# Performance work log

Hardware: AMD Instinct MI355X
Metric: run time of the kernel (lower is better)

Reference implementation:

```python
import jax, jax.numpy as jnp
import numpy as np

D_MODEL = 1024
N_HEADS = 16
LATENT_HEADS = 8
LATENT_DIM = 512
N_LATENTS = 64
WINDOW = 256
HEAD_DIM = D_MODEL // N_HEADS          # 64
LAT_HD = LATENT_DIM // LATENT_HEADS    # 64
B, S = 2, 4096


def setup_inputs() -> dict:
    key = jax.random.key(0)
    ks = jax.random.split(key, 11)
    std = 0.02
    w = lambda k, shp: jax.random.normal(k, shp, jnp.float32) * std
    return {
        'x': jax.random.normal(ks[0], (B, S, D_MODEL), jnp.float32),
        'wq': w(ks[1], (D_MODEL, D_MODEL)),
        'wk': w(ks[2], (D_MODEL, D_MODEL)),
        'wv': w(ks[3], (D_MODEL, D_MODEL)),
        'wgq': w(ks[4], (D_MODEL, LATENT_DIM)),
        'wgk': w(ks[5], (D_MODEL, LATENT_DIM)),
        'wgv': w(ks[6], (D_MODEL, LATENT_DIM)),
        'r_out_w': w(ks[7], (LATENT_DIM, D_MODEL)),
        'gate_local_w': w(ks[8], (N_HEADS, HEAD_DIM)),
        'gate_remote_w': w(ks[9], (N_HEADS, HEAD_DIM)),
        'w_out': w(ks[10], (D_MODEL, D_MODEL)),
    }


def _pool_to_latents(x):
    # x: [B, S, C]; S assumed divisible by N_LATENTS (matches torch path when S % chunk == 0)
    Bx, Sx, C = x.shape
    chunk = max(1, Sx // N_LATENTS)
    return x.reshape(Bx, N_LATENTS, chunk, C).mean(axis=2)  # [B, Nl, C]


def _local_window_attn(Q, K, V):
    # causal sliding-window attention: query i attends keys in [i-WINDOW+1, i]
    Bx, H, Sx, D = Q.shape
    W = WINDOW
    nb = Sx // W
    Qb = Q.reshape(Bx, H, nb, W, D)
    # pad one leading block of keys/values so block b sees key blocks (b-1, b)
    Kp = jnp.pad(K, ((0, 0), (0, 0), (W, 0), (0, 0))).reshape(Bx, H, nb + 1, W, D)
    Vp = jnp.pad(V, ((0, 0), (0, 0), (W, 0), (0, 0))).reshape(Bx, H, nb + 1, W, D)
    Kw = jnp.concatenate([Kp[:, :, :-1], Kp[:, :, 1:]], axis=3)  # [B,H,nb,2W,D]
    Vw = jnp.concatenate([Vp[:, :, :-1], Vp[:, :, 1:]], axis=3)
    i = jnp.arange(W)[:, None]
    j = jnp.arange(2 * W)[None, :]
    # key_pos <= q_pos  <=> j <= i+W ; key_pos >= q_pos-W+1 <=> j > i
    base = (j > i) & (j <= i + W)                       # [W, 2W]
    blk0 = (jnp.arange(nb) > 0)[:, None, None] | (j >= W)[None, :, :]  # pad keys invalid in block 0
    mask = base[None, :, :] & blk0                      # [nb, W, 2W]
    sc = jnp.einsum('bhnid,bhnjd->bhnij', Qb, Kw) / np.sqrt(D).astype(np.float32)
    sc = jnp.where(mask[None, None], sc, -jnp.inf)
    p = jax.nn.softmax(sc, axis=-1)
    out = jnp.einsum('bhnij,bhnjd->bhnid', p, Vw)
    return out.reshape(Bx, H, Sx, D)


def reference(x, wq, wk, wv, wgq, wgk, wgv, r_out_w, gate_local_w, gate_remote_w, w_out):
    Bx, Sx, _ = x.shape
    chunk = max(1, Sx // N_LATENTS)
    # local path projections: [B, H, S, Dh]
    Q = (x @ wq).reshape(Bx, Sx, N_HEADS, HEAD_DIM).transpose(0, 2, 1, 3)
    K = (x @ wk).reshape(Bx, Sx, N_HEADS, HEAD_DIM).transpose(0, 2, 1, 3)
    V = (x @ wv).reshape(Bx, Sx, N_HEADS, HEAD_DIM).transpose(0, 2, 1, 3)
    local = _local_window_attn(Q, K, V)                 # [B, H, S, Dh]
    # latent (remote) path: GQ over mean-pooled latents, chunk-causal
    GQ = (x @ wgq).reshape(Bx, Sx, LATENT_HEADS, LAT_HD).transpose(0, 2, 1, 3)   # [B,Lh,S,Ld]
    GK = _pool_to_latents(x @ wgk).reshape(Bx, N_LATENTS, LATENT_HEADS, LAT_HD).transpose(0, 2, 1, 3)
    GV = _pool_to_latents(x @ wgv).reshape(Bx, N_LATENTS, LATENT_HEADS, LAT_HD).transpose(0, 2, 1, 3)
    lsc = jnp.einsum('bhsd,bhnd->bhsn', GQ, GK) / np.sqrt(LAT_HD).astype(np.float32)
    lmask = jnp.arange(N_LATENTS)[None, :] <= (jnp.arange(Sx) // chunk)[:, None]  # [S, Nl]
    lsc = jnp.where(lmask[None, None], lsc, -jnp.inf)
    lp = jax.nn.softmax(lsc, axis=-1)
    rem = jnp.einsum('bhsn,bhnd->bhsd', lp, GV)          # [B, Lh, S, Ld]
    rem = rem.transpose(0, 2, 1, 3).reshape(Bx, Sx, LATENT_DIM) @ r_out_w  # [B, S, d_model]
    rem = rem.reshape(Bx, Sx, N_HEADS, HEAD_DIM).transpose(0, 2, 1, 3)     # [B, H, S, Dh]
    # learned per-head gates computed from the query
    gl = jax.nn.sigmoid(jnp.einsum('bhsd,hd->bhs', Q, gate_local_w))[..., None]
    gr = jax.nn.sigmoid(jnp.einsum('bhsd,hd->bhs', Q, gate_remote_w))[..., None]
    out = gl * local + gr * rem                          # [B, H, S, Dh]
    out = out.transpose(0, 2, 1, 3).reshape(Bx, Sx, D_MODEL)
    return out @ w_out
```

## Files before the change

kernel.cpp:

```cpp
#include <hip/hip_runtime.h>

#define AS1 __attribute__((address_space(1)))
#define AS3 __attribute__((address_space(3)))

typedef float    f32x4  __attribute__((ext_vector_type(4)));
typedef __bf16   bf16x8 __attribute__((ext_vector_type(8)));
typedef __bf16   bf16x4 __attribute__((ext_vector_type(4)));
typedef unsigned int u32x4 __attribute__((ext_vector_type(4)));

static constexpr int SEQ = 4096, NBATCH = 2, DMODEL = 1024, NHEADS = 16, HDIM = 64;
static constexpr int LHEADS = 8, LDIM = 512, NLAT = 64, WIN = 256;
static constexpr int BSROWS = NBATCH * SEQ;
static constexpr int QKVN = 3584;
static constexpr int KOFF = 1024, VOFF = 2048, GQOFF = 3072;

struct TJ { const float* in; __bf16* out; int K; int N; };
struct TJ8 { TJ j[8]; };
__global__ __launch_bounds__(256) void prep_all(const float* __restrict__ x,
                                                __bf16* __restrict__ xb,
                                                __bf16* __restrict__ xpool, TJ8 jobs) {
    __shared__ float tbuf[32][33];
    int bid = blockIdx.x, t = threadIdx.x;
    if (bid < 512) {
        int bn = bid >> 2;
        int c  = (bid & 3) * 256 + t;
        const float* p = x + (size_t)bn * 64 * 1024 + c;
        __bf16* q = xb + (size_t)bn * 64 * 1024 + c;
        float s = 0.f;
        #pragma unroll 8
        for (int j = 0; j < 64; ++j) {
            float v = p[(size_t)j * 1024];
            q[(size_t)j * 1024] = (__bf16)v;
            s += v;
        }
        xpool[(size_t)bn * 1024 + c] = (__bf16)(s * 0.015625f);
    } else if (bid < 8704) {
        int ti = bid - 512;
        TJ jb = jobs.j[ti >> 10];
        int rem = ti & 1023;
        int k0 = (rem >> 5) * 32, n0 = (rem & 31) * 32;
        if (k0 >= jb.K || n0 >= jb.N) return;
        int tx = t & 31, ty = t >> 5;
        #pragma unroll
        for (int i = ty; i < 32; i += 8) tbuf[i][tx] = jb.in[(size_t)(k0 + i) * jb.N + n0 + tx];
        __syncthreads();
        #pragma unroll
        for (int i = ty; i < 32; i += 8) jb.out[(size_t)(n0 + i) * jb.K + k0 + tx] = (__bf16)tbuf[tx][i];
    } else {
        int zi = bid - 8704;
        size_t idx = ((size_t)zi * 256 + t) * 16;
        u32x4 z = {0u, 0u, 0u, 0u};
        *(u32x4*)(xpool + 128 * 1024 + idx)     = z;
        *(u32x4*)(xpool + 128 * 1024 + idx + 8) = z;
    }
}

#define BAR() do { __builtin_amdgcn_sched_barrier(0); __builtin_amdgcn_s_barrier(); \
                   __builtin_amdgcn_sched_barrier(0); } while (0)
#define LGK0() do { asm volatile("s_waitcnt lgkmcnt(0)" ::: "memory"); \
                    __builtin_amdgcn_sched_barrier(0); } while (0)
#define VMC(n) do { asm volatile("s_waitcnt vmcnt(" #n ")" ::: "memory"); \
                    __builtin_amdgcn_sched_barrier(0); } while (0)
#define STG(gp, regionbase, rowbase, ktc) do { \
    int row_ = (rowbase) + (t >> 3); \
    int tc_ = (t & 7) ^ ((t >> 3) & 7); \
    __builtin_amdgcn_global_load_lds( \
        (const AS1 void*)((gp) + (size_t)row_ * K + (ktc) + tc_ * 8), \
        (AS3 void*)(lds + (regionbase) + (rowbase) * 128 + w * 1024), 16, 0, 0); \
} while (0)
#define LOADA(buf, qm) do { \
    _Pragma("unroll") for (int ai_ = 0; ai_ < 4; ++ai_) \
    _Pragma("unroll") for (int ks_ = 0; ks_ < 2; ++ks_) \
        a[ai_][ks_] = *(const bf16x8*)(lds + ((((buf) * 65536) + \
            (wm * 128 + (qm) * 64 + ai_ * 16 + l15) * 128 + ks_ * 64 + l4 * 16) ^ rswz)); \
} while (0)
#define LOADB2(buf, half) do { \
    _Pragma("unroll") for (int j_ = 0; j_ < 2; ++j_) \
    _Pragma("unroll") for (int ks_ = 0; ks_ < 2; ++ks_) \
        b2[j_][ks_] = *(const bf16x8*)(lds + ((((buf) * 65536 + 32768) + \
            (wn * 64 + ((half) * 2 + j_) * 16 + l15) * 128 + ks_ * 64 + l4 * 16) ^ rswz)); \
} while (0)
#define MFMA_PH(qm, half) do { \
    __builtin_amdgcn_s_setprio(1); \
    _Pragma("unroll") for (int ai_ = 0; ai_ < 4; ++ai_) \
    _Pragma("unroll") for (int j_ = 0; j_ < 2; ++j_) { \
        f32x4 c_ = acc[(qm) * 4 + ai_][(half) * 2 + j_]; \
        c_ = __builtin_amdgcn_mfma_f32_16x16x32_bf16(a[ai_][0], b2[j_][0], c_, 0, 0, 0); \
        c_ = __builtin_amdgcn_mfma_f32_16x16x32_bf16(a[ai_][1], b2[j_][1], c_, 0, 0, 0); \
        acc[(qm) * 4 + ai_][(half) * 2 + j_] = c_; \
    } \
    __builtin_amdgcn_s_setprio(0); \
} while (0)

__global__ __launch_bounds__(512, 2) void gemm256_bf16(
    const __bf16* __restrict__ A, const __bf16* __restrict__ Bt,
    int M, int N, int K, __bf16* __restrict__ outb, __bf16* __restrict__ Vt,
    const __bf16* __restrict__ A2, const __bf16* __restrict__ B2,
    __bf16* __restrict__ out2) {
    __shared__ char lds[131072];
    const int t = threadIdx.x, w = t >> 6, l = t & 63;
    const int wm = w >> 2, wn = w & 3;
    const int l15 = l & 15, l4 = l >> 4;
    const int NT = K >> 6;
    const int rswz = (l15 & 7) << 4;

    const __bf16* Ab; const __bf16* Bb; __bf16* outp; int Nout, m0, n0; bool doVt;
    if (blockIdx.y == 14) {
        if (blockIdx.x >= 4) return;
        m0 = 0; n0 = blockIdx.x * 256;
        Ab = A2; Bb = B2 + (size_t)n0 * K;
        outp = out2; Nout = 1024; doVt = false;
    } else {
        m0 = blockIdx.x * 256; n0 = blockIdx.y * 256;
        Ab = A + (size_t)m0 * K; Bb = Bt + (size_t)n0 * K;
        outp = outb; Nout = N; doVt = (n0 >= VOFF && n0 < GQOFF);
    }

    f32x4 acc[8][4];
    #pragma unroll
    for (int i = 0; i < 8; ++i)
        #pragma unroll
        for (int j = 0; j < 4; ++j) acc[i][j] = (f32x4){0.f, 0.f, 0.f, 0.f};
    bf16x8 a[4][2], b2[2][2];

    STG(Ab, 0, 0, 0);        STG(Ab, 0, 128, 0);
    STG(Ab, 0, 64, 0);       STG(Ab, 0, 192, 0);
    STG(Bb, 32768, 0, 0);    STG(Bb, 32768, 64, 0);
    STG(Bb, 32768, 128, 0);  STG(Bb, 32768, 192, 0);
    STG(Ab, 65536, 0, 64);   STG(Ab, 65536, 128, 64);
    VMC(2); BAR();

    int it = 0;
    for (; it + 3 < NT; it += 2) {
        const int kt1 = (it + 1) << 6, kt2 = (it + 2) << 6, kt3 = (it + 3) << 6;
        LOADA(0, 0); LOADB2(0, 0);
        STG(Ab, 65536, 64, kt1); STG(Ab, 65536, 192, kt1);
        BAR(); LGK0(); MFMA_PH(0, 0); BAR();
        LOADB2(0, 1);
        STG(Bb, 98304, 0, kt1); STG(Bb, 98304, 64, kt1);
        BAR(); LGK0(); MFMA_PH(0, 1); BAR();
        LOADA(0, 1); LOADB2(0, 0);
        STG(Bb, 98304, 128, kt1); STG(Bb, 98304, 192, kt1);
        BAR(); LGK0(); MFMA_PH(1, 0); BAR();
        LOADB2(0, 1);
        STG(Ab, 0, 0, kt2); STG(Ab, 0, 128, kt2);
        BAR(); LGK0(); MFMA_PH(1, 1); VMC(2); BAR();
        LOADA(1, 0); LOADB2(1, 0);
        STG(Ab, 0, 64, kt2); STG(Ab, 0, 192, kt2);
        BAR(); LGK0(); MFMA_PH(0, 0); BAR();
        LOADB2(1, 1);
        STG(Bb, 32768, 0, kt2); STG(Bb, 32768, 64, kt2);
        BAR(); LGK0(); MFMA_PH(0, 1); BAR();
        LOADA(1, 1); LOADB2(1, 0);
        STG(Bb, 32768, 128, kt2); STG(Bb, 32768, 192, kt2);
        BAR(); LGK0(); MFMA_PH(1, 0); BAR();
        LOADB2(1, 1);
        STG(Ab, 65536, 0, kt3); STG(Ab, 65536, 128, kt3);
        BAR(); LGK0(); MFMA_PH(1, 1); VMC(2); BAR();
    }
    {
        const int kt1 = (it + 1) << 6;
        LOADA(0, 0); LOADB2(0, 0);
        STG(Ab, 65536, 64, kt1); STG(Ab, 65536, 192, kt1);
        BAR(); LGK0(); MFMA_PH(0, 0); BAR();
        LOADB2(0, 1);
        STG(Bb, 98304, 0, kt1); STG(Bb, 98304, 64, kt1);
        BAR(); LGK0(); MFMA_PH(0, 1); BAR();
        LOADA(0, 1); LOADB2(0, 0);
        STG(Bb, 98304, 128, kt1); STG(Bb, 98304, 192, kt1);
        BAR(); LGK0(); MFMA_PH(1, 0); BAR();
        LOADB2(0, 1);
        BAR(); LGK0(); MFMA_PH(1, 1); VMC(0); BAR();
        LOADA(1, 0); LOADB2(1, 0);
        BAR(); LGK0(); MFMA_PH(0, 0); BAR();
        LOADB2(1, 1);
        BAR(); LGK0(); MFMA_PH(0, 1); BAR();
        LOADA(1, 1); LOADB2(1, 0);
        BAR(); LGK0(); MFMA_PH(1, 0); BAR();
        LOADB2(1, 1);
        LGK0(); MFMA_PH(1, 1);
    }

    int cr = l4 * 4, cc = l15;
    if (doVt) {
        #pragma unroll
        for (int mi = 0; mi < 8; ++mi) {
            #pragma unroll
            for (int ni = 0; ni < 4; ++ni) {
                int vcol = (n0 - VOFF) + wn * 64 + ni * 16 + cc;
                int row0 = m0 + wm * 128 + mi * 16 + cr;
                int bb = row0 >> 12, ss = row0 & 4095;
                bf16x4 pk;
                #pragma unroll
                for (int r = 0; r < 4; ++r) pk[r] = (__bf16)acc[mi][ni][r];
                *(bf16x4*)(Vt + ((size_t)bb * DMODEL + vcol) * SEQ + ss) = pk;
            }
        }
    } else {
        #pragma unroll
        for (int mi = 0; mi < 8; ++mi) {
            #pragma unroll
            for (int ni = 0; ni < 4; ++ni) {
                int col = n0 + wn * 64 + ni * 16 + cc;
                #pragma unroll
                for (int r = 0; r < 4; ++r) {
                    int row = m0 + wm * 128 + mi * 16 + cr + r;
                    outp[(size_t)row * Nout + col] = (__bf16)acc[mi][ni][r];
                }
            }
        }
    }
}
#undef LOADA
#undef LOADB2
#undef MFMA_PH

#define LOADA3(base, qm) do { \
    _Pragma("unroll") for (int ai_ = 0; ai_ < 2; ++ai_) \
    _Pragma("unroll") for (int ks_ = 0; ks_ < 2; ++ks_) \
        a[ai_][ks_] = *(const bf16x8*)(lds + (((base) + \
            (wm2 * 64 + (qm) * 32 + ai_ * 16 + l15) * 128 + ks_ * 64 + l4 * 16) ^ rswz)); \
} while (0)
#define LOADB3(base, nh) do { \
    _Pragma("unroll") for (int j_ = 0; j_ < 2; ++j_) \
    _Pragma("unroll") for (int ks_ = 0; ks_ < 2; ++ks_) \
        b2[j_][ks_] = *(const bf16x8*)(lds + (((base) + 16384 + \
            (wn * 64 + (nh) * 32 + j_ * 16 + l15) * 128 + ks_ * 64 + l4 * 16) ^ rswz)); \
} while (0)
#define MFMA_P3(qm, nh) do { \
    __builtin_amdgcn_s_setprio(1); \
    _Pragma("unroll") for (int ai_ = 0; ai_ < 2; ++ai_) \
    _Pragma("unroll") for (int j_ = 0; j_ < 2; ++j_) { \
        f32x4 c_ = acc[(qm) * 2 + ai_][(nh) * 2 + j_]; \
        c_ = __builtin_amdgcn_mfma_f32_16x16x32_bf16(a[ai_][0], b2[j_][0], c_, 0, 0, 0); \
        c_ = __builtin_amdgcn_mfma_f32_16x16x32_bf16(a[ai_][1], b2[j_][1], c_, 0, 0, 0); \
        acc[(qm) * 2 + ai_][(nh) * 2 + j_] = c_; \
    } \
    __builtin_amdgcn_s_setprio(0); \
} while (0)

template <bool EPI, bool OUTBF>
__global__ __launch_bounds__(512, 1) void gemm128n(
    const __bf16* __restrict__ A, const __bf16* __restrict__ Bt,
    int M, int N, int K,
    __bf16* __restrict__ outb, float* __restrict__ outf,
    const __bf16* __restrict__ lcl, const float* __restrict__ grb) {
    __shared__ char lds[147456];
    const int t = threadIdx.x, w = t >> 6, l = t & 63;
    const int wm2 = w >> 2, wn = w & 3;
    const int l15 = l & 15, l4 = l >> 4;
    const int m0 = blockIdx.x * 128, n0 = blockIdx.y * 256;
    const int NT = K >> 6;
    const int rswz = (l15 & 7) << 4;

    f32x4 acc[4][4];
    #pragma unroll
    for (int i = 0; i < 4; ++i)
        #pragma unroll
        for (int j = 0; j < 4; ++j) acc[i][j] = (f32x4){0.f, 0.f, 0.f, 0.f};
    bf16x8 a[2][2], b2[2][2];

    const __bf16* Ab = A + (size_t)m0 * K;
    const __bf16* Bb = Bt + (size_t)n0 * K;

    STG(Ab, 0, 0, 0);      STG(Ab, 0, 64, 0);
    STG(Bb, 16384, 0, 0);  STG(Bb, 16384, 64, 0);
    STG(Bb, 16384, 128, 0); STG(Bb, 16384, 192, 0);
    STG(Ab, 49152, 0, 64);      STG(Ab, 49152, 64, 64);
    STG(Bb, 65536, 0, 64);  STG(Bb, 65536, 64, 64);
    STG(Bb, 65536, 128, 64); STG(Bb, 65536, 192, 64);
    VMC(6); BAR();

    int cb = 0, nb = 98304;
    for (int it = 0; it + 2 < NT; ++it) {
        const int kt2 = (it + 2) << 6;
        LOADA3(cb, 0); LOADB3(cb, 0);
        STG(Ab, nb, 0, kt2); STG(Ab, nb, 64, kt2);
        BAR(); LGK0(); MFMA_P3(0, 0); BAR();
        LOADB3(cb, 1);
        STG(Bb, nb + 16384, 0, kt2); STG(Bb, nb + 16384, 64, kt2);
        BAR(); LGK0(); MFMA_P3(0, 1); BAR();
        LOADA3(cb, 1); LOADB3(cb, 0);
        STG(Bb, nb + 16384, 128, kt2); STG(Bb, nb + 16384, 192, kt2);
        BAR(); LGK0(); MFMA_P3(1, 0); BAR();
        LOADB3(cb, 1);
        BAR(); LGK0(); MFMA_P3(1, 1); VMC(6); BAR();
        cb = (cb == 98304) ? 0 : cb + 49152;
        nb = (nb == 98304) ? 0 : nb + 49152;
    }
    {
        LOADA3(cb, 0); LOADB3(cb, 0);
        BAR(); LGK0(); MFMA_P3(0, 0); BAR();
        LOADB3(cb, 1);
        BAR(); LGK0(); MFMA_P3(0, 1); BAR();
        LOADA3(cb, 1); LOADB3(cb, 0);
        BAR(); LGK0(); MFMA_P3(1, 0); BAR();
        LOADB3(cb, 1);
        BAR(); LGK0(); MFMA_P3(1, 1); VMC(0); BAR();
        cb = (cb == 98304) ? 0 : cb + 49152;
    }
    {
        LOADA3(cb, 0); LOADB3(cb, 0);
        BAR(); LGK0(); MFMA_P3(0, 0); BAR();
        LOADB3(cb, 1);
        BAR(); LGK0(); MFMA_P3(0, 1); BAR();
        LOADA3(cb, 1); LOADB3(cb, 0);
        BAR(); LGK0(); MFMA_P3(1, 0); BAR();
        LOADB3(cb, 1);
        LGK0(); MFMA_P3(1, 1);
    }

    int cr = l4 * 4, cc = l15;
    #pragma unroll
    for (int mi = 0; mi < 4; ++mi) {
        #pragma unroll
        for (int ni = 0; ni < 4; ++ni) {
            int col = n0 + wn * 64 + ni * 16 + cc;
            #pragma unroll
            for (int r = 0; r < 4; ++r) {
                int row = m0 + wm2 * 64 + mi * 16 + cr + r;
                float v = acc[mi][ni][r];
                if constexpr (EPI) {
                    v = (float)lcl[(size_t)row * 1024 + col] +
                        grb[(size_t)row * 16 + (col >> 6)] * v;
                }
                if constexpr (OUTBF) outb[(size_t)row * N + col] = (__bf16)v;
                else                 outf[(size_t)row * N + col] = v;
            }
        }
    }
}
#undef BAR
#undef LGK0
#undef VMC
#undef STG
#undef LOADA3
#undef LOADB3
#undef MFMA_P3

__global__ __launch_bounds__(256, 2) void attn_fused(
    const __bf16* __restrict__ QKVG, const __bf16* __restrict__ Vt,
    const __bf16* __restrict__ GKV,
    const float* __restrict__ glw, const float* __restrict__ grw,
    __bf16* __restrict__ outl, float* __restrict__ grbuf,
    __bf16* __restrict__ rem) {
    __shared__ alignas(16) char smem[32768];
    int t = threadIdx.x, w = t >> 6, l = t & 63;
    int l15 = l & 15, l4 = l >> 4;
    int b = blockIdx.z;
    f32x4 zero = {0.f, 0.f, 0.f, 0.f};

    if (blockIdx.y < 16) {
        int blk = blockIdx.x, h = blockIdx.y;
        char* sPb = smem;

        bf16x8 qf[4][2];
        long qbase = (long)b * SEQ + blk * 256 + 64 * w;
        #pragma unroll
        for (int qq = 0; qq < 4; ++qq)
            #pragma unroll
            for (int ks = 0; ks < 2; ++ks)
                qf[qq][ks] = *(const bf16x8*)(QKVG + (size_t)(qbase + qq * 16 + l15) * QKVN
                                              + h * 64 + ks * 32 + l4 * 8);

        float dlp[4], drp[4];
        #pragma unroll
        for (int qq = 0; qq < 4; ++qq) {
            float dl = 0.f, dr = 0.f;
            #pragma unroll
            for (int ks = 0; ks < 2; ++ks) {
                const float* gp = glw + h * 64 + ks * 32 + l4 * 8;
                const float* rp = grw + h * 64 + ks * 32 + l4 * 8;
                #pragma unroll
                for (int j = 0; j < 8; ++j) {
                    float qv = (float)qf[qq][ks][j];
                    dl += qv * gp[j];
                    dr += qv * rp[j];
                }
            }
            dlp[qq] = dl; drp[qq] = dr;
        }
        float glv[4], grv[4];
        #pragma unroll
        for (int qq = 0; qq < 4; ++qq) {
            float dl = dlp[qq] + __shfl_xor(dlp[qq], 16);
            dl += __shfl_xor(dl, 32);
            float dr = drp[qq] + __shfl_xor(drp[qq], 16);
            dr += __shfl_xor(dr, 32);
            glv[qq] = 1.f / (1.f + __expf(-dl));
            grv[qq] = 1.f / (1.f + __expf(-dr));
        }
        if (l4 == 0) {
            #pragma unroll
            for (int qq = 0; qq < 4; ++qq)
                grbuf[(size_t)(qbase + qq * 16 + l15) * 16 + h] = grv[qq];
        }

        f32x4 acc[4][4];
        #pragma unroll
        for (int a2 = 0; a2 < 4; ++a2)
            #pragma unroll
            for (int d = 0; d < 4; ++d) acc[a2][d] = zero;
        float psum[4] = {0.f, 0.f, 0.f, 0.f};

        char* sPw = sPb + w * 4096;
        int nsteps = (w == 3) ? 10 : 11;
        int kk0 = 64 * w;
        long g0 = (long)b * SEQ + (long)(blk - 1) * WIN;
        const __bf16* vtb = Vt + (size_t)b * DMODEL * SEQ + (size_t)(h * 64) * SEQ;

        for (int stp = 0; stp < nsteps; ++stp) {
            int kk = kk0 + 32 * stp;
            f32x4 sacc[2][4];
            #pragma unroll
            for (int kt2 = 0; kt2 < 2; ++kt2) {
                int krow = kk + kt2 * 16 + l15;
                long kgrow = g0 + krow;
                if (blk == 0 && krow < 256) kgrow = (long)b * SEQ;
                const __bf16* kp = QKVG + (size_t)kgrow * QKVN + KOFF + h * 64;
                bf16x8 af0 = *(const bf16x8*)(kp + l4 * 8);
                bf16x8 af1 = *(const bf16x8*)(kp + 32 + l4 * 8);
                #pragma unroll
                for (int qq = 0; qq < 4; ++qq) {
                    f32x4 s = __builtin_amdgcn_mfma_f32_16x16x32_bf16(af0, qf[qq][0], zero, 0, 0, 0);
                    sacc[kt2][qq] = __builtin_amdgcn_mfma_f32_16x16x32_bf16(af1, qf[qq][1], s, 0, 0, 0);
                }
            }
            #pragma unroll
            for (int qq = 0; qq < 4; ++qq) {
                int qloc = 64 * w + qq * 16 + l15;
                int prow = qq * 16 + l15;
                #pragma unroll
                for (int kt2 = 0; kt2 < 2; ++kt2) {
                    int jb = kk + kt2 * 16 + l4 * 4;
                    bf16x4 pb;
                    #pragma unroll
                    for (int r = 0; r < 4; ++r) {
                        int jw = jb + r;
                        bool act = (jw > qloc) && (jw <= qloc + 256) && (blk > 0 || jw >= 256);
                        float pv = act ? __expf(sacc[kt2][qq][r] * 0.125f) : 0.f;
                        psum[qq] += pv;
                        pb[r] = (__bf16)pv;
                    }
                    *(bf16x4*)(sPw + prow * 64 + ((kt2 * 32 + l4 * 8) ^ ((prow & 3) << 4))) = pb;
                }
            }
            int kglob = (blk - 1) * WIN + kk + l4 * 8;
            if (kglob < 0) kglob = 0;
            bf16x8 pa[4], bv[4];
            #pragma unroll
            for (int qq = 0; qq < 4; ++qq) {
                int prow = qq * 16 + l15;
                pa[qq] = *(const bf16x8*)(sPw + prow * 64 + ((l4 * 16) ^ ((prow & 3) << 4)));
            }
            #pragma unroll
            for (int dt = 0; dt < 4; ++dt)
                bv[dt] = *(const bf16x8*)(vtb + (size_t)(dt * 16 + l15) * SEQ + kglob);
            #pragma unroll
            for (int qq = 0; qq < 4; ++qq)
                #pragma unroll
                for (int dt = 0; dt < 4; ++dt)
                    acc[qq][dt] = __builtin_amdgcn_mfma_f32_16x16x32_bf16(pa[qq], bv[dt], acc[qq][dt], 0, 0, 0);
        }

        float cmb[4];
        #pragma unroll
        for (int qq = 0; qq < 4; ++qq) {
            float s = psum[qq] + __shfl_xor(psum[qq], 16);
            s += __shfl_xor(s, 32);
            cmb[qq] = glv[qq] / s;
        }
        #pragma unroll
        for (int qq = 0; qq < 4; ++qq) {
            #pragma unroll
            for (int r = 0; r < 4; ++r) {
                float sc = __shfl(cmb[qq], l4 * 4 + r, 64);
                size_t row = (size_t)(qbase + qq * 16 + l4 * 4 + r);
                __bf16* op = outl + row * DMODEL + h * 64 + l15;
                #pragma unroll
                for (int dt = 0; dt < 4; ++dt)
                    op[dt * 16] = (__bf16)(acc[qq][dt][r] * sc);
            }
        }
    } else {
        int sb = blockIdx.x, lh = blockIdx.y - 16;
        char* sK  = smem;
        char* sVt = smem + 8192;
        char* sPb = smem + 16384;

        bf16x8 qf[4][2];
        long qbase = (long)b * SEQ + sb * 256 + 64 * w;
        #pragma unroll
        for (int qq = 0; qq < 4; ++qq)
            #pragma unroll
            for (int ks = 0; ks < 2; ++ks)
                qf[qq][ks] = *(const bf16x8*)(QKVG + (size_t)(qbase + qq * 16 + l15) * QKVN
                                              + GQOFF + lh * 64 + ks * 32 + l4 * 8);

        #pragma unroll
        for (int rep = 0; rep < 2; ++rep) {
            int ci = rep * 256 + t;
            int row = ci >> 3, c8 = (ci & 7) * 8;
            u32x4 kv = *(const u32x4*)(GKV + (size_t)(b * 64 + row) * 1024 + lh * 64 + c8);
            *(u32x4*)(sK + row * 128 + ((c8 * 2) ^ ((row & 7) << 4))) = kv;
        }
        #pragma unroll
        for (int rep = 0; rep < 16; ++rep) {
            int idx = rep * 256 + t;
            int d = idx & 63, n = idx >> 6;
            __bf16 v = GKV[(size_t)(b * 64 + n) * 1024 + 512 + lh * 64 + d];
            *(__bf16*)(sVt + d * 128 + ((n * 2) ^ ((d & 7) << 4))) = v;
        }
        __syncthreads();

        f32x4 acc[4][4];
        #pragma unroll
        for (int a2 = 0; a2 < 4; ++a2)
            #pragma unroll
            for (int d = 0; d < 4; ++d) acc[a2][d] = zero;
        float psum[4] = {0.f, 0.f, 0.f, 0.f};

        char* sPw = sPb + w * 4096;
        int qloc0 = sb * 256 + 64 * w;

        #pragma unroll
        for (int stp = 0; stp < 2; ++stp) {
            int kk = 32 * stp;
            f32x4 sacc[2][4];
            #pragma unroll
            for (int kt2 = 0; kt2 < 2; ++kt2) {
                int krow = kk + kt2 * 16 + l15;
                int swz = (krow & 7) << 4;
                bf16x8 af0 = *(const bf16x8*)(sK + krow * 128 + ((l4 * 16) ^ swz));
                bf16x8 af1 = *(const bf16x8*)(sK + krow * 128 + ((64 + l4 * 16) ^ swz));
                #pragma unroll
                for (int qq = 0; qq < 4; ++qq) {
                    f32x4 s = __builtin_amdgcn_mfma_f32_16x16x32_bf16(af0, qf[qq][0], zero, 0, 0, 0);
                    sacc[kt2][qq] = __builtin_amdgcn_mfma_f32_16x16x32_bf16(af1, qf[qq][1], s, 0, 0, 0);
                }
            }
            #pragma unroll
            for (int qq = 0; qq < 4; ++qq) {
                int qdv = (qloc0 + qq * 16 + l15) >> 6;
                int prow = qq * 16 + l15;
                #pragma unroll
                for (int kt2 = 0; kt2 < 2; ++kt2) {
                    int nb = kk + kt2 * 16 + l4 * 4;
                    bf16x4 pb;
                    #pragma unroll
                    for (int r = 0; r < 4; ++r) {
                        int n = nb + r;
                        float pv = (n <= qdv) ? __expf(sacc[kt2][qq][r] * 0.125f) : 0.f;
                        psum[qq] += pv;
                        pb[r] = (__bf16)pv;
                    }
                    *(bf16x4*)(sPw + prow * 64 + ((kt2 * 32 + l4 * 8) ^ ((prow & 3) << 4))) = pb;
                }
            }
            bf16x8 pa[4], bv[4];
            #pragma unroll
            for (int qq = 0; qq < 4; ++qq) {
                int prow = qq * 16 + l15;
                pa[qq] = *(const bf16x8*)(sPw + prow * 64 + ((l4 * 16) ^ ((prow & 3) << 4)));
            }
            #pragma unroll
            for (int dt = 0; dt < 4; ++dt) {
                int d = dt * 16 + l15;
                bv[dt] = *(const bf16x8*)(sVt + d * 128 + ((kk * 2 + l4 * 16) ^ ((d & 7) << 4)));
            }
            #pragma unroll
            for (int qq = 0; qq < 4; ++qq)
                #pragma unroll
                for (int dt = 0; dt < 4; ++dt)
                    acc[qq][dt] = __builtin_amdgcn_mfma_f32_16x16x32_bf16(pa[qq], bv[dt], acc[qq][dt], 0, 0, 0);
        }

        float cmb[4];
        #pragma unroll
        for (int qq = 0; qq < 4; ++qq) {
            float s = psum[qq] + __shfl_xor(psum[qq], 16);
            s += __shfl_xor(s, 32);
            cmb[qq] = 1.f / s;
        }
        #pragma unroll
        for (int qq = 0; qq < 4; ++qq) {
            #pragma unroll
            for (int r = 0; r < 4; ++r) {
                float sc = __shfl(cmb[qq], l4 * 4 + r, 64);
                size_t row = (size_t)(qbase + qq * 16 + l4 * 4 + r);
                __bf16* op = rem + row * LDIM + lh * 64 + l15;
                #pragma unroll
                for (int dt = 0; dt < 4; ++dt)
                    op[dt * 16] = (__bf16)(acc[qq][dt][r] * sc);
            }
        }
    }
}

extern "C" void kernel_launch(void* const* d_in, const int* in_sizes, int n_in,
                              void* d_out, int out_size, void* d_ws, size_t ws_size,
                              hipStream_t stream) {
    (void)in_sizes; (void)n_in; (void)out_size; (void)ws_size;
    const float* x    = (const float*)d_in[0];
    const float* wq   = (const float*)d_in[1];
    const float* wk   = (const float*)d_in[2];
    const float* wv   = (const float*)d_in[3];
    const float* wgq  = (const float*)d_in[4];
    const float* wgk  = (const float*)d_in[5];
    const float* wgv  = (const float*)d_in[6];
    const float* rout = (const float*)d_in[7];
    const float* glw  = (const float*)d_in[8];
    const float* grw  = (const float*)d_in[9];
    const float* wout = (const float*)d_in[10];

    char* p = (char*)d_ws;
    auto alloc = [&](size_t bytes) {
        char* r = p;
        p += (bytes + 255) & ~(size_t)255;
        return r;
    };
    __bf16* xb    = (__bf16*)alloc((size_t)BSROWS * DMODEL * 2);
    __bf16* QKVG  = (__bf16*)alloc((size_t)BSROWS * QKVN * 2);
    __bf16* VtG   = (__bf16*)alloc((size_t)BSROWS * DMODEL * 2);
    __bf16* wcatT = (__bf16*)alloc((size_t)QKVN * DMODEL * 2);
    __bf16* woutT = (__bf16*)alloc((size_t)DMODEL * DMODEL * 2);
    __bf16* wgkvT = (__bf16*)alloc((size_t)1024 * DMODEL * 2);
    __bf16* routT = (__bf16*)alloc((size_t)DMODEL * LDIM * 2);
    __bf16* xpool = (__bf16*)alloc((size_t)256 * DMODEL * 2);
    __bf16* GKVb  = (__bf16*)alloc((size_t)256 * 1024 * 2);
    __bf16* localg= (__bf16*)alloc((size_t)BSROWS * DMODEL * 2);
    float*  grbuf = (float*) alloc((size_t)BSROWS * 16 * 4);
    __bf16* remb  = (__bf16*)alloc((size_t)BSROWS * LDIM * 2);
    __bf16* outpre = xb;

    TJ8 jobs;
    jobs.j[0] = {wq,   wcatT,                 DMODEL, DMODEL};
    jobs.j[1] = {wk,   wcatT + 1024 * DMODEL, DMODEL, DMODEL};
    jobs.j[2] = {wv,   wcatT + 2048 * DMODEL, DMODEL, DMODEL};
    jobs.j[3] = {wgq,  wcatT + 3072 * DMODEL, DMODEL, LDIM};
    jobs.j[4] = {wout, woutT,                 DMODEL, DMODEL};
    jobs.j[5] = {wgk,  wgkvT,                 DMODEL, LDIM};
    jobs.j[6] = {wgv,  wgkvT + 512 * DMODEL,  DMODEL, LDIM};
    jobs.j[7] = {rout, routT,                 LDIM,   DMODEL};

    prep_all<<<dim3(512 + 8192 + 32), 256, 0, stream>>>(x, xb, xpool, jobs);

    gemm256_bf16<<<dim3(32, 15), 512, 0, stream>>>(xb, wcatT, BSROWS, QKVN, DMODEL,
                                                   QKVG, VtG, xpool, wgkvT, GKVb);

    attn_fused<<<dim3(16, 24, 2), 256, 0, stream>>>(QKVG, VtG, GKVb, glw, grw,
                                                    localg, grbuf, remb);

    gemm128n<true, true><<<dim3(64, 4), 512, 0, stream>>>(remb, routT, BSROWS, DMODEL, LDIM, outpre, nullptr, localg, grbuf);
    gemm128n<false, false><<<dim3(64, 4), 512, 0, stream>>>(outpre, woutT, BSROWS, DMODEL, DMODEL, nullptr, (float*)d_out, nullptr, nullptr);
}
```

Before: 170.0 us.

## Restructure gemm128n inner loop into two phases with full A fragment reuse

The gemm128n main loop goes from four sub-phases per K tile to two. Each wave now loads all four A fragments once and reuses them across both B halves, which halves the barrier count per iteration and cuts redundant A LDS reads. The global-to-LDS staging is redistributed across the two phases. This raises register pressure from the larger A fragment array and gives less interleaving between loads and MFMAs. Separately, attn_fused launch bounds move from 2 to 3 blocks per CU, which may force register spills.

```diff
diff --git a/kernel.cpp b/kernel.cpp
--- a/kernel.cpp
+++ b/kernel.cpp
@@ -215,11 +215,11 @@
 #undef LOADB2
 #undef MFMA_PH
 
-#define LOADA3(base, qm) do { \
-    _Pragma("unroll") for (int ai_ = 0; ai_ < 2; ++ai_) \
+#define LOADA3F(base) do { \
+    _Pragma("unroll") for (int ai_ = 0; ai_ < 4; ++ai_) \
     _Pragma("unroll") for (int ks_ = 0; ks_ < 2; ++ks_) \
         a[ai_][ks_] = *(const bf16x8*)(lds + (((base) + \
-            (wm2 * 64 + (qm) * 32 + ai_ * 16 + l15) * 128 + ks_ * 64 + l4 * 16) ^ rswz)); \
+            (wm2 * 64 + ai_ * 16 + l15) * 128 + ks_ * 64 + l4 * 16) ^ rswz)); \
 } while (0)
 #define LOADB3(base, nh) do { \
     _Pragma("unroll") for (int j_ = 0; j_ < 2; ++j_) \
@@ -227,14 +227,14 @@
         b2[j_][ks_] = *(const bf16x8*)(lds + (((base) + 16384 + \
             (wn * 64 + (nh) * 32 + j_ * 16 + l15) * 128 + ks_ * 64 + l4 * 16) ^ rswz)); \
 } while (0)
-#define MFMA_P3(qm, nh) do { \
+#define MFMA_P3N(nh) do { \
     __builtin_amdgcn_s_setprio(1); \
-    _Pragma("unroll") for (int ai_ = 0; ai_ < 2; ++ai_) \
+    _Pragma("unroll") for (int ai_ = 0; ai_ < 4; ++ai_) \
     _Pragma("unroll") for (int j_ = 0; j_ < 2; ++j_) { \
-        f32x4 c_ = acc[(qm) * 2 + ai_][(nh) * 2 + j_]; \
+        f32x4 c_ = acc[ai_][(nh) * 2 + j_]; \
         c_ = __builtin_amdgcn_mfma_f32_16x16x32_bf16(a[ai_][0], b2[j_][0], c_, 0, 0, 0); \
         c_ = __builtin_amdgcn_mfma_f32_16x16x32_bf16(a[ai_][1], b2[j_][1], c_, 0, 0, 0); \
-        acc[(qm) * 2 + ai_][(nh) * 2 + j_] = c_; \
+        acc[ai_][(nh) * 2 + j_] = c_; \
     } \
     __builtin_amdgcn_s_setprio(0); \
 } while (0)
@@ -258,7 +258,7 @@
     for (int i = 0; i < 4; ++i)
         #pragma unroll
         for (int j = 0; j < 4; ++j) acc[i][j] = (f32x4){0.f, 0.f, 0.f, 0.f};
-    bf16x8 a[2][2], b2[2][2];
+    bf16x8 a[4][2], b2[2][2];
 
     const __bf16* Ab = A + (size_t)m0 * K;
     const __bf16* Bb = Bt + (size_t)n0 * K;
@@ -274,40 +274,27 @@
     int cb = 0, nb = 98304;
     for (int it = 0; it + 2 < NT; ++it) {
         const int kt2 = (it + 2) << 6;
-        LOADA3(cb, 0); LOADB3(cb, 0);
-        STG(Ab, nb, 0, kt2); STG(Ab, nb, 64, kt2);
-        BAR(); LGK0(); MFMA_P3(0, 0); BAR();
+        LOADA3F(cb); LOADB3(cb, 0);
+        STG(Ab, nb, 0, kt2); STG(Ab, nb, 64, kt2); STG(Bb, nb + 16384, 0, kt2);
+        BAR(); LGK0(); MFMA_P3N(0); BAR();
         LOADB3(cb, 1);
-        STG(Bb, nb + 16384, 0, kt2); STG(Bb, nb + 16384, 64, kt2);
-        BAR(); LGK0(); MFMA_P3(0, 1); BAR();
-        LOADA3(cb, 1); LOADB3(cb, 0);
-        STG(Bb, nb + 16384, 128, kt2); STG(Bb, nb + 16384, 192, kt2);
-        BAR(); LGK0(); MFMA_P3(1, 0); BAR();
-        LOADB3(cb, 1);
-        BAR(); LGK0(); MFMA_P3(1, 1); VMC(6); BAR();
+        STG(Bb, nb + 16384, 64, kt2); STG(Bb, nb + 16384, 128, kt2); STG(Bb, nb + 16384, 192, kt2);
+        BAR(); LGK0(); MFMA_P3N(1); VMC(6); BAR();
         cb = (cb == 98304) ? 0 : cb + 49152;
         nb = (nb == 98304) ? 0 : nb + 49152;
     }
     {
-        LOADA3(cb, 0); LOADB3(cb, 0);
-        BAR(); LGK0(); MFMA_P3(0, 0); BAR();
+        LOADA3F(cb); LOADB3(cb, 0);
+        BAR(); LGK0(); MFMA_P3N(0); BAR();
         LOADB3(cb, 1);
-        BAR(); LGK0(); MFMA_P3(0, 1); BAR();
-        LOADA3(cb, 1); LOADB3(cb, 0);
-        BAR(); LGK0(); MFMA_P3(1, 0); BAR();
+        BAR(); LGK0(); MFMA_P3N(1); VMC(0); BAR();
+        cb = (cb == 98304) ? 0 : cb + 49152;
+    }
+    {
+        LOADA3F(cb); LOADB3(cb, 0);
+        BAR(); LGK0(); MFMA_P3N(0); BAR();
         LOADB3(cb, 1);
-        BAR(); LGK0(); MFMA_P3(1, 1); VMC(0); BAR();
-        cb = (cb == 98304) ? 0 : cb + 49152;
-    }
-    {
-        LOADA3(cb, 0); LOADB3(cb, 0);
-        BAR(); LGK0(); MFMA_P3(0, 0); BAR();
-        LOADB3(cb, 1);
-        BAR(); LGK0(); MFMA_P3(0, 1); BAR();
-        LOADA3(cb, 1); LOADB3(cb, 0);
-        BAR(); LGK0(); MFMA_P3(1, 0); BAR();
-        LOADB3(cb, 1);
-        LGK0(); MFMA_P3(1, 1);
+        LGK0(); MFMA_P3N(1);
     }
 
     int cr = l4 * 4, cc = l15;
@@ -334,11 +321,11 @@
 #undef LGK0
 #undef VMC
 #undef STG
-#undef LOADA3
+#undef LOADA3F
 #undef LOADB3
-#undef MFMA_P3
-
-__global__ __launch_bounds__(256, 2) void attn_fused(
+#undef MFMA_P3N
+
+__global__ __launch_bounds__(256, 3) void attn_fused(
     const __bf16* __restrict__ QKVG, const __bf16* __restrict__ Vt,
     const __bf16* __restrict__ GKV,
     const float* __restrict__ glw, const float* __restrict__ grw,
```

New measurement: 183.3 us. 7.8% more time.
